# Kernel tuning notes

Measured on AMD Instinct MI355X. Metric: run time of the kernel, lower is better.

## Reference

```python
import jax, jax.numpy as jnp
import numpy as np

B, H, S, D = 2, 16, 2048, 64

def setup_inputs() -> dict:
    key0 = jax.random.key(0)
    kq, kk, kv = jax.random.split(key0, 3)
    return {
        "query": jax.random.normal(kq, (B, H, S, D), dtype=jnp.float32),
        "key": jax.random.normal(kk, (B, H, S, D), dtype=jnp.float32),
        "value": jax.random.normal(kv, (B, H, S, D), dtype=jnp.float32),
        "inv_scale_factor": jnp.full((1,), np.sqrt(D), dtype=jnp.float32),
    }

def reference(query, key, value, inv_scale_factor):
    # qk: [B,H,S,S]
    qk = jnp.einsum("bhqd,bhkd->bhqk", query, key)
    scaled_qk = qk / inv_scale_factor
    softmax_qk = jax.nn.softmax(scaled_qk, axis=-1)
    # dropout_p = 0.0 -> identity (deterministic reference)
    out = jnp.einsum("bhqk,bhkd->bhqd", softmax_qk, value)
    return out
```

## Files before the change

kernel.cpp:

```cpp
#include <hip/hip_runtime.h>
#include <hip/hip_bf16.h>


typedef __attribute__((ext_vector_type(8))) short short8;
typedef __attribute__((ext_vector_type(4))) float floatx4;

#define NB 2
#define NH 16
#define SS 2048
#define DD 64

#define QM 64
#define KN 64
#define NITER (SS / KN)

#define LOG2E 1.44269504f

#define MFMA16(a, b, c) __builtin_amdgcn_mfma_f32_16x16x32_bf16(a, b, c, 0, 0, 0)
#define WAIT_LGKM0() __builtin_amdgcn_s_waitcnt(0x007F)

#define KF_SHORTS (32 * 32 * 2 * 2 * 2 * 64 * 8)
#define VF_SHORTS (32 * 32 * 2 * 4 * 64 * 8)

static __device__ inline unsigned pack2bf(float a, float b) {
    unsigned ua = __builtin_bit_cast(unsigned, a) + 0x8000u;
    unsigned ub = __builtin_bit_cast(unsigned, b) + 0x8000u;
    return __builtin_amdgcn_perm(ub, ua, 0x07060302u);
}

static __device__ inline unsigned cvtpk(float lo, float hi) {
    unsigned r;
    asm("v_cvt_pk_bf16_f32 %0, %1, %2" : "=v"(r) : "v"(lo), "v"(hi));
    return r;
}

static __device__ inline int swz(int row, int col) {
    return row * 64 + ((((col >> 3) ^ row) & 7) << 3) + (col & 7);
}

__global__ __launch_bounds__(256)
void prepack_kernel(const float* __restrict__ K, const float* __restrict__ V,
                    short* __restrict__ Kf, short* __restrict__ Vf)
{
    int t = blockIdx.x * 256 + threadIdx.x;
    if (t < 524288) {
        int lane = t & 63, rest = t >> 6;
        int ks = rest & 1, nt = (rest >> 1) & 1, wn = (rest >> 2) & 1;
        int hk = rest >> 3;
        int n_g = hk * 64 + wn * 32 + nt * 16 + (lane & 15);
        int d   = ks * 32 + ((lane >> 4) << 3);
        const float* src = K + (size_t)n_g * DD + d;
        float4 f0 = *(const float4*)src;
        float4 f1 = *(const float4*)(src + 4);
        uint4 o;
        o.x = pack2bf(f0.x, f0.y); o.y = pack2bf(f0.z, f0.w);
        o.z = pack2bf(f1.x, f1.y); o.w = pack2bf(f1.z, f1.w);
        *(uint4*)(Kf + (size_t)t * 8) = o;
    } else {
        int u = t - 524288;
        int lane = u & 63, rest = u >> 6;
        int dt = rest & 3, wn = (rest >> 2) & 1;
        int hk = rest >> 3;
        int d  = dt * 16 + (lane & 15);
        int n0 = hk * 64 + wn * 32 + ((lane >> 4) << 3);
        const float* src = V + (size_t)n0 * DD + d;
        float v[8];
#pragma unroll
        for (int jj = 0; jj < 8; ++jj) v[jj] = src[(size_t)jj * DD];
        uint4 o;
        o.x = pack2bf(v[0], v[1]); o.y = pack2bf(v[2], v[3]);
        o.z = pack2bf(v[4], v[5]); o.w = pack2bf(v[6], v[7]);
        *(uint4*)(Vf + (size_t)u * 8) = o;
    }
}

__global__ __launch_bounds__(256, 4)
void fattn_kernel(const float* __restrict__ Q, const short* __restrict__ Kf,
                  const short* __restrict__ Vf, const float* __restrict__ isf,
                  float* __restrict__ O)
{
    __shared__ __align__(16) char smem[17664];
    short* P_lds = (short*)smem;
    float* O_buf = (float*)smem;
    float* l_buf = (float*)(smem + 17408);
#define OSTR 68

    const int tid  = threadIdx.x;
    const int wave = tid >> 6;
    const int w_m  = wave & 1;
    const int w_n  = wave >> 1;
    const int lane = tid & 63;
    const int l15  = lane & 15;
    const int quad = lane >> 4;

    const int b    = blockIdx.x & 1023;
    const int xcd  = b & 7;
    const int j    = b >> 3;
    const int head = xcd + 8 * (j & 3);
    const int qt   = j >> 2;

    const float scl2 = (1.0f / isf[0]) * LOG2E;

    const float* Qh = Q + (size_t)head * SS * DD;
    float*       Oh = O + (size_t)head * SS * DD;

    const short* kp = Kf + (size_t)head * 131072 + w_n * 2048 + lane * 8;
    const short* vp = Vf + (size_t)head * 131072 + w_n * 2048 + lane * 8;

    short8 kA0 = *(const short8*)(kp + 0);
    short8 kA1 = *(const short8*)(kp + 512);
    short8 kA2 = *(const short8*)(kp + 1024);
    short8 kA3 = *(const short8*)(kp + 1536);
    short8 kB0, kB1, kB2, kB3;

    short8 q_frag[2][2];
#pragma unroll
    for (int mt = 0; mt < 2; ++mt) {
        const float* qrow = Qh + (size_t)(qt * QM + w_m * 32 + mt * 16 + l15) * DD;
#pragma unroll
        for (int ks = 0; ks < 2; ++ks) {
            float4 f0 = *(const float4*)(qrow + ks * 32 + quad * 8);
            float4 f1 = *(const float4*)(qrow + ks * 32 + quad * 8 + 4);
            uint4 qp;
            qp.x = pack2bf(f0.x * scl2, f0.y * scl2);
            qp.y = pack2bf(f0.z * scl2, f0.w * scl2);
            qp.z = pack2bf(f1.x * scl2, f1.y * scl2);
            qp.w = pack2bf(f1.z * scl2, f1.w * scl2);
            q_frag[mt][ks] = __builtin_bit_cast(short8, qp);
        }
    }

    floatx4 o_acc[2][4];
#pragma unroll
    for (int mt = 0; mt < 2; ++mt)
#pragma unroll
        for (int dt = 0; dt < 4; ++dt)
#pragma unroll
            for (int i = 0; i < 4; ++i) o_acc[mt][dt][i] = 0.0f;

    float lsum[2] = {0.0f, 0.0f};

    short* pw[2][2];
    const short* pr[2];
#pragma unroll
    for (int mt = 0; mt < 2; ++mt) {
        const int m = w_m * 32 + mt * 16 + l15;
#pragma unroll
        for (int nt = 0; nt < 2; ++nt)
            pw[mt][nt] = &P_lds[swz(m, w_n * 32 + nt * 16 + quad * 4)];
        pr[mt] = &P_lds[swz(m, w_n * 32 + quad * 8)];
    }

#define SOFTMAX_ST(sv, mt, nt)                                        \
    do {                                                              \
        float p0 = __builtin_amdgcn_exp2f((sv)[0]);                   \
        float p1 = __builtin_amdgcn_exp2f((sv)[1]);                   \
        float p2 = __builtin_amdgcn_exp2f((sv)[2]);                   \
        float p3 = __builtin_amdgcn_exp2f((sv)[3]);                   \
        uint2 pk; pk.x = cvtpk(p0, p1); pk.y = cvtpk(p2, p3);         \
        *(uint2*)pw[mt][nt] = pk;                                     \
        lsum[mt] += (p0 + p1) + (p2 + p3);                            \
    } while (0)

#define FATTN_BODY(K0, K1, K2, K3, V0, V1, V2, V3)                    \
    do {                                                              \
        floatx4 s00 = {0.f, 0.f, 0.f, 0.f};                           \
        floatx4 s01 = s00, s10 = s00, s11 = s00;                      \
        s00 = MFMA16(K0, q_frag[0][0], s00);                          \
        s10 = MFMA16(K0, q_frag[1][0], s10);                          \
        s01 = MFMA16(K2, q_frag[0][0], s01);                          \
        s11 = MFMA16(K2, q_frag[1][0], s11);                          \
        s00 = MFMA16(K1, q_frag[0][1], s00);                          \
        s10 = MFMA16(K1, q_frag[1][1], s10);                          \
        s01 = MFMA16(K3, q_frag[0][1], s01);                          \
        s11 = MFMA16(K3, q_frag[1][1], s11);                          \
        SOFTMAX_ST(s00, 0, 0);                                        \
        SOFTMAX_ST(s10, 1, 0);                                        \
        SOFTMAX_ST(s01, 0, 1);                                        \
        SOFTMAX_ST(s11, 1, 1);                                        \
        WAIT_LGKM0();    \
        short8 pf0 = *(const short8*)pr[0];                           \
        short8 pf1 = *(const short8*)pr[1];                           \
        o_acc[0][0] = MFMA16(V0, pf0, o_acc[0][0]);                   \
        o_acc[0][1] = MFMA16(V1, pf0, o_acc[0][1]);                   \
        o_acc[0][2] = MFMA16(V2, pf0, o_acc[0][2]);                   \
        o_acc[0][3] = MFMA16(V3, pf0, o_acc[0][3]);                   \
        o_acc[1][0] = MFMA16(V0, pf1, o_acc[1][0]);                   \
        o_acc[1][1] = MFMA16(V1, pf1, o_acc[1][1]);                   \
        o_acc[1][2] = MFMA16(V2, pf1, o_acc[1][2]);                   \
        o_acc[1][3] = MFMA16(V3, pf1, o_acc[1][3]);                   \
    } while (0)

    for (int kb = 0; kb < NITER; kb += 2) {
        short8 v0 = *(const short8*)(vp + 0);
        short8 v1 = *(const short8*)(vp + 512);
        short8 v2 = *(const short8*)(vp + 1024);
        short8 v3 = *(const short8*)(vp + 1536);
        kB0 = *(const short8*)(kp + 4096);
        kB1 = *(const short8*)(kp + 4608);
        kB2 = *(const short8*)(kp + 5120);
        kB3 = *(const short8*)(kp + 5632);
        FATTN_BODY(kA0, kA1, kA2, kA3, v0, v1, v2, v3);

        short8 w0 = *(const short8*)(vp + 4096);
        short8 w1 = *(const short8*)(vp + 4608);
        short8 w2 = *(const short8*)(vp + 5120);
        short8 w3 = *(const short8*)(vp + 5632);
        kA0 = *(const short8*)(kp + 8192);
        kA1 = *(const short8*)(kp + 8704);
        kA2 = *(const short8*)(kp + 9216);
        kA3 = *(const short8*)(kp + 9728);
        FATTN_BODY(kB0, kB1, kB2, kB3, w0, w1, w2, w3);

        kp += 8192; vp += 8192;
    }

#pragma unroll
    for (int mt = 0; mt < 2; ++mt) {
        lsum[mt] += __shfl_xor(lsum[mt], 16);
        lsum[mt] += __shfl_xor(lsum[mt], 32);
    }
    __syncthreads();

    if (w_n == 1) {
#pragma unroll
        for (int mt = 0; mt < 2; ++mt) {
            const int orow = (w_m * 32 + mt * 16 + l15) * OSTR;
#pragma unroll
            for (int dt = 0; dt < 4; ++dt) {
                float4 v = { o_acc[mt][dt][0], o_acc[mt][dt][1],
                             o_acc[mt][dt][2], o_acc[mt][dt][3] };
                *(float4*)&O_buf[orow + dt * 16 + quad * 4] = v;
            }
            if (quad == 0) l_buf[w_m * 32 + mt * 16 + l15] = lsum[mt];
        }
    }
    __syncthreads();
    if (w_n == 0) {
#pragma unroll
        for (int mt = 0; mt < 2; ++mt) {
            const int m_blk = w_m * 32 + mt * 16 + l15;
            float lt = lsum[mt] + l_buf[m_blk];
            float rl = 1.0f / lt;
            float* orow = Oh + (size_t)(qt * QM + m_blk) * DD;
#pragma unroll
            for (int dt = 0; dt < 4; ++dt) {
                float4 part = *(float4*)&O_buf[m_blk * OSTR + dt * 16 + quad * 4];
                float4 v;
                v.x = (o_acc[mt][dt][0] + part.x) * rl;
                v.y = (o_acc[mt][dt][1] + part.y) * rl;
                v.z = (o_acc[mt][dt][2] + part.z) * rl;
                v.w = (o_acc[mt][dt][3] + part.w) * rl;
                *(float4*)(orow + dt * 16 + quad * 4) = v;
            }
        }
    }
}

extern "C" void kernel_launch(void* const* d_in, const int* in_sizes, int n_in,
                              void* d_out, int out_size, void* d_ws, size_t ws_size,
                              hipStream_t stream) {
    const float* Q   = (const float*)d_in[0];
    const float* K   = (const float*)d_in[1];
    const float* V   = (const float*)d_in[2];
    const float* isf = (const float*)d_in[3];
    float* O = (float*)d_out;

    short* Kf = (short*)d_ws;
    short* Vf = Kf + KF_SHORTS;

    prepack_kernel<<<4096, 256, 0, stream>>>(K, V, Kf, Vf);
    fattn_kernel<<<1024, 256, 0, stream>>>(Q, Kf, Vf, isf, O);
}
```

Measured before the change: 139.5 us.

## Switch attention to 32x32x16 MFMA and pass P through lane shuffles instead of LDS

```diff
diff --git a/kernel.cpp b/kernel.cpp
--- a/kernel.cpp
+++ b/kernel.cpp
@@ -3,24 +3,17 @@
 
 
 typedef __attribute__((ext_vector_type(8))) short short8;
-typedef __attribute__((ext_vector_type(4))) float floatx4;
-
-#define NB 2
-#define NH 16
+typedef __attribute__((ext_vector_type(16))) float floatx16;
+
 #define SS 2048
 #define DD 64
-
-#define QM 64
-#define KN 64
-#define NITER (SS / KN)
-
+#define NITER (SS / 64)
 #define LOG2E 1.44269504f
 
-#define MFMA16(a, b, c) __builtin_amdgcn_mfma_f32_16x16x32_bf16(a, b, c, 0, 0, 0)
-#define WAIT_LGKM0() __builtin_amdgcn_s_waitcnt(0x007F)
-
-#define KF_SHORTS (32 * 32 * 2 * 2 * 2 * 64 * 8)
-#define VF_SHORTS (32 * 32 * 2 * 4 * 64 * 8)
+#define MFMA32(a, b, c) __builtin_amdgcn_mfma_f32_32x32x16_bf16(a, b, c, 0, 0, 0)
+
+#define KF_SHORTS (32 * 64 * 4 * 64 * 8)
+#define VF_SHORTS (32 * 64 * 4 * 64 * 8)
 
 static __device__ inline unsigned pack2bf(float a, float b) {
     unsigned ua = __builtin_bit_cast(unsigned, a) + 0x8000u;
@@ -32,10 +25,6 @@
     unsigned r;
     asm("v_cvt_pk_bf16_f32 %0, %1, %2" : "=v"(r) : "v"(lo), "v"(hi));
     return r;
-}
-
-static __device__ inline int swz(int row, int col) {
-    return row * 64 + ((((col >> 3) ^ row) & 7) << 3) + (col & 7);
 }
 
 __global__ __launch_bounds__(256)
@@ -43,13 +32,13 @@
                     short* __restrict__ Kf, short* __restrict__ Vf)
 {
     int t = blockIdx.x * 256 + threadIdx.x;
+    int lane = t & 63;
+    int l31 = lane & 31, hi = lane >> 5;
     if (t < 524288) {
-        int lane = t & 63, rest = t >> 6;
-        int ks = rest & 1, nt = (rest >> 1) & 1, wn = (rest >> 2) & 1;
-        int hk = rest >> 3;
-        int n_g = hk * 64 + wn * 32 + nt * 16 + (lane & 15);
-        int d   = ks * 32 + ((lane >> 4) << 3);
-        const float* src = K + (size_t)n_g * DD + d;
+        int c = t >> 6;
+        int ks = c & 3, kvb = (c >> 2) & 63, hd = c >> 8;
+        const float* src = K + (size_t)hd * 131072
+                             + (size_t)(kvb * 32 + l31) * 64 + ks * 16 + hi * 8;
         float4 f0 = *(const float4*)src;
         float4 f1 = *(const float4*)(src + 4);
         uint4 o;
@@ -58,15 +47,14 @@
         *(uint4*)(Kf + (size_t)t * 8) = o;
     } else {
         int u = t - 524288;
-        int lane = u & 63, rest = u >> 6;
-        int dt = rest & 3, wn = (rest >> 2) & 1;
-        int hk = rest >> 3;
-        int d  = dt * 16 + (lane & 15);
-        int n0 = hk * 64 + wn * 32 + ((lane >> 4) << 3);
-        const float* src = V + (size_t)n0 * DD + d;
+        int c = u >> 6;
+        int ksl = c & 1, dt = (c >> 1) & 1, kvb = (c >> 2) & 63, hd = c >> 8;
+        const float* src = V + (size_t)hd * 131072
+                             + (size_t)(kvb * 32 + ksl * 16 + hi * 8) * 64
+                             + dt * 32 + l31;
         float v[8];
 #pragma unroll
-        for (int jj = 0; jj < 8; ++jj) v[jj] = src[(size_t)jj * DD];
+        for (int jj = 0; jj < 8; ++jj) v[jj] = src[(size_t)jj * 64];
         uint4 o;
         o.x = pack2bf(v[0], v[1]); o.y = pack2bf(v[2], v[3]);
         o.z = pack2bf(v[4], v[5]); o.w = pack2bf(v[6], v[7]);
@@ -80,7 +68,6 @@
                   float* __restrict__ O)
 {
     __shared__ __align__(16) char smem[17664];
-    short* P_lds = (short*)smem;
     float* O_buf = (float*)smem;
     float* l_buf = (float*)(smem + 17408);
 #define OSTR 68
@@ -90,8 +77,8 @@
     const int w_m  = wave & 1;
     const int w_n  = wave >> 1;
     const int lane = tid & 63;
-    const int l15  = lane & 15;
-    const int quad = lane >> 4;
+    const int l31  = lane & 31;
+    const int hi   = lane >> 5;
 
     const int b    = blockIdx.x & 1023;
     const int xcd  = b & 7;
@@ -113,147 +100,117 @@
     short8 kA3 = *(const short8*)(kp + 1536);
     short8 kB0, kB1, kB2, kB3;
 
-    short8 q_frag[2][2];
-#pragma unroll
-    for (int mt = 0; mt < 2; ++mt) {
-        const float* qrow = Qh + (size_t)(qt * QM + w_m * 32 + mt * 16 + l15) * DD;
-#pragma unroll
-        for (int ks = 0; ks < 2; ++ks) {
-            float4 f0 = *(const float4*)(qrow + ks * 32 + quad * 8);
-            float4 f1 = *(const float4*)(qrow + ks * 32 + quad * 8 + 4);
+    short8 q_frag[4];
+    {
+        const float* qrow = Qh + (size_t)(qt * 64 + w_m * 32 + l31) * DD;
+#pragma unroll
+        for (int ks = 0; ks < 4; ++ks) {
+            float4 f0 = *(const float4*)(qrow + ks * 16 + hi * 8);
+            float4 f1 = *(const float4*)(qrow + ks * 16 + hi * 8 + 4);
             uint4 qp;
             qp.x = pack2bf(f0.x * scl2, f0.y * scl2);
             qp.y = pack2bf(f0.z * scl2, f0.w * scl2);
             qp.z = pack2bf(f1.x * scl2, f1.y * scl2);
             qp.w = pack2bf(f1.z * scl2, f1.w * scl2);
-            q_frag[mt][ks] = __builtin_bit_cast(short8, qp);
+            q_frag[ks] = __builtin_bit_cast(short8, qp);
         }
     }
 
-    floatx4 o_acc[2][4];
-#pragma unroll
-    for (int mt = 0; mt < 2; ++mt)
-#pragma unroll
-        for (int dt = 0; dt < 4; ++dt)
-#pragma unroll
-            for (int i = 0; i < 4; ++i) o_acc[mt][dt][i] = 0.0f;
-
-    float lsum[2] = {0.0f, 0.0f};
-
-    short* pw[2][2];
-    const short* pr[2];
-#pragma unroll
-    for (int mt = 0; mt < 2; ++mt) {
-        const int m = w_m * 32 + mt * 16 + l15;
-#pragma unroll
-        for (int nt = 0; nt < 2; ++nt)
-            pw[mt][nt] = &P_lds[swz(m, w_n * 32 + nt * 16 + quad * 4)];
-        pr[mt] = &P_lds[swz(m, w_n * 32 + quad * 8)];
-    }
-
-#define SOFTMAX_ST(sv, mt, nt)                                        \
-    do {                                                              \
-        float p0 = __builtin_amdgcn_exp2f((sv)[0]);                   \
-        float p1 = __builtin_amdgcn_exp2f((sv)[1]);                   \
-        float p2 = __builtin_amdgcn_exp2f((sv)[2]);                   \
-        float p3 = __builtin_amdgcn_exp2f((sv)[3]);                   \
-        uint2 pk; pk.x = cvtpk(p0, p1); pk.y = cvtpk(p2, p3);         \
-        *(uint2*)pw[mt][nt] = pk;                                     \
-        lsum[mt] += (p0 + p1) + (p2 + p3);                            \
+    floatx16 o_acc[2];
+#pragma unroll
+    for (int i = 0; i < 16; ++i) { o_acc[0][i] = 0.0f; o_acc[1][i] = 0.0f; }
+    float lsum = 0.0f;
+
+#define FBODY(K0, K1, K2, K3, V00, V01, V10, V11)                          \
+    do {                                                                   \
+        floatx16 s = {0.f,0.f,0.f,0.f,0.f,0.f,0.f,0.f,                     \
+                      0.f,0.f,0.f,0.f,0.f,0.f,0.f,0.f};                    \
+        s = MFMA32(K0, q_frag[0], s);                                      \
+        s = MFMA32(K1, q_frag[1], s);                                      \
+        s = MFMA32(K2, q_frag[2], s);                                      \
+        s = MFMA32(K3, q_frag[3], s);                                      \
+        float p[16];                                                       \
+        _Pragma("unroll")                                                  \
+        for (int i = 0; i < 16; ++i) p[i] = __builtin_amdgcn_exp2f(s[i]);  \
+        lsum += (((p[0]+p[1])+(p[2]+p[3]))+((p[4]+p[5])+(p[6]+p[7])))      \
+              + (((p[8]+p[9])+(p[10]+p[11]))+((p[12]+p[13])+(p[14]+p[15])));\
+         \
+        unsigned x0 = cvtpk(p[0], p[1]),   x1 = cvtpk(p[2], p[3]);         \
+        unsigned y0 = cvtpk(p[4], p[5]),   y1 = cvtpk(p[6], p[7]);         \
+        unsigned x2 = cvtpk(p[8], p[9]),   x3 = cvtpk(p[10], p[11]);       \
+        unsigned y2 = cvtpk(p[12], p[13]), y3 = cvtpk(p[14], p[15]);       \
+                              \
+        unsigned f0 = __shfl_xor(hi ? x0 : y0, 32);                        \
+        unsigned f1 = __shfl_xor(hi ? x1 : y1, 32);                        \
+        unsigned f2 = __shfl_xor(hi ? x2 : y2, 32);                        \
+        unsigned f3 = __shfl_xor(hi ? x3 : y3, 32);                        \
+        uint4 B0u = { hi ? f0 : x0, hi ? f1 : x1,                          \
+                      hi ? y0 : f0, hi ? y1 : f1 };    \
+        uint4 B1u = { hi ? f2 : x2, hi ? f3 : x3,                          \
+                      hi ? y2 : f2, hi ? y3 : f3 };   \
+        short8 Bf0 = __builtin_bit_cast(short8, B0u);                      \
+        short8 Bf1 = __builtin_bit_cast(short8, B1u);                      \
+        o_acc[0] = MFMA32(V00, Bf0, o_acc[0]);                             \
+        o_acc[1] = MFMA32(V10, Bf0, o_acc[1]);                             \
+        o_acc[0] = MFMA32(V01, Bf1, o_acc[0]);                             \
+        o_acc[1] = MFMA32(V11, Bf1, o_acc[1]);                             \
     } while (0)
 
-#define FATTN_BODY(K0, K1, K2, K3, V0, V1, V2, V3)                    \
-    do {                                                              \
-        floatx4 s00 = {0.f, 0.f, 0.f, 0.f};                           \
-        floatx4 s01 = s00, s10 = s00, s11 = s00;                      \
-        s00 = MFMA16(K0, q_frag[0][0], s00);                          \
-        s10 = MFMA16(K0, q_frag[1][0], s10);                          \
-        s01 = MFMA16(K2, q_frag[0][0], s01);                          \
-        s11 = MFMA16(K2, q_frag[1][0], s11);                          \
-        s00 = MFMA16(K1, q_frag[0][1], s00);                          \
-        s10 = MFMA16(K1, q_frag[1][1], s10);                          \
-        s01 = MFMA16(K3, q_frag[0][1], s01);                          \
-        s11 = MFMA16(K3, q_frag[1][1], s11);                          \
-        SOFTMAX_ST(s00, 0, 0);                                        \
-        SOFTMAX_ST(s10, 1, 0);                                        \
-        SOFTMAX_ST(s01, 0, 1);                                        \
-        SOFTMAX_ST(s11, 1, 1);                                        \
-        WAIT_LGKM0();    \
-        short8 pf0 = *(const short8*)pr[0];                           \
-        short8 pf1 = *(const short8*)pr[1];                           \
-        o_acc[0][0] = MFMA16(V0, pf0, o_acc[0][0]);                   \
-        o_acc[0][1] = MFMA16(V1, pf0, o_acc[0][1]);                   \
-        o_acc[0][2] = MFMA16(V2, pf0, o_acc[0][2]);                   \
-        o_acc[0][3] = MFMA16(V3, pf0, o_acc[0][3]);                   \
-        o_acc[1][0] = MFMA16(V0, pf1, o_acc[1][0]);                   \
-        o_acc[1][1] = MFMA16(V1, pf1, o_acc[1][1]);                   \
-        o_acc[1][2] = MFMA16(V2, pf1, o_acc[1][2]);                   \
-        o_acc[1][3] = MFMA16(V3, pf1, o_acc[1][3]);                   \
-    } while (0)
-
     for (int kb = 0; kb < NITER; kb += 2) {
-        short8 v0 = *(const short8*)(vp + 0);
-        short8 v1 = *(const short8*)(vp + 512);
-        short8 v2 = *(const short8*)(vp + 1024);
-        short8 v3 = *(const short8*)(vp + 1536);
+        short8 v00 = *(const short8*)(vp + 0);
+        short8 v01 = *(const short8*)(vp + 512);
+        short8 v10 = *(const short8*)(vp + 1024);
+        short8 v11 = *(const short8*)(vp + 1536);
         kB0 = *(const short8*)(kp + 4096);
         kB1 = *(const short8*)(kp + 4608);
         kB2 = *(const short8*)(kp + 5120);
         kB3 = *(const short8*)(kp + 5632);
-        FATTN_BODY(kA0, kA1, kA2, kA3, v0, v1, v2, v3);
-
-        short8 w0 = *(const short8*)(vp + 4096);
-        short8 w1 = *(const short8*)(vp + 4608);
-        short8 w2 = *(const short8*)(vp + 5120);
-        short8 w3 = *(const short8*)(vp + 5632);
+        FBODY(kA0, kA1, kA2, kA3, v00, v01, v10, v11);
+
+        short8 w00 = *(const short8*)(vp + 4096);
+        short8 w01 = *(const short8*)(vp + 4608);
+        short8 w10 = *(const short8*)(vp + 5120);
+        short8 w11 = *(const short8*)(vp + 5632);
         kA0 = *(const short8*)(kp + 8192);
         kA1 = *(const short8*)(kp + 8704);
         kA2 = *(const short8*)(kp + 9216);
         kA3 = *(const short8*)(kp + 9728);
-        FATTN_BODY(kB0, kB1, kB2, kB3, w0, w1, w2, w3);
+        FBODY(kB0, kB1, kB2, kB3, w00, w01, w10, w11);
 
         kp += 8192; vp += 8192;
     }
 
-#pragma unroll
-    for (int mt = 0; mt < 2; ++mt) {
-        lsum[mt] += __shfl_xor(lsum[mt], 16);
-        lsum[mt] += __shfl_xor(lsum[mt], 32);
-    }
-    __syncthreads();
-
+    lsum += __shfl_xor(lsum, 32);
+
+    const int row = w_m * 32 + l31;
     if (w_n == 1) {
 #pragma unroll
-        for (int mt = 0; mt < 2; ++mt) {
-            const int orow = (w_m * 32 + mt * 16 + l15) * OSTR;
-#pragma unroll
-            for (int dt = 0; dt < 4; ++dt) {
-                float4 v = { o_acc[mt][dt][0], o_acc[mt][dt][1],
-                             o_acc[mt][dt][2], o_acc[mt][dt][3] };
-                *(float4*)&O_buf[orow + dt * 16 + quad * 4] = v;
+        for (int dt = 0; dt < 2; ++dt)
+#pragma unroll
+            for (int g = 0; g < 4; ++g) {
+                float4 v = { o_acc[dt][g * 4 + 0], o_acc[dt][g * 4 + 1],
+                             o_acc[dt][g * 4 + 2], o_acc[dt][g * 4 + 3] };
+                *(float4*)&O_buf[row * OSTR + dt * 32 + g * 8 + hi * 4] = v;
             }
-            if (quad == 0) l_buf[w_m * 32 + mt * 16 + l15] = lsum[mt];
-        }
+        if (lane < 32) l_buf[row] = lsum;
     }
     __syncthreads();
     if (w_n == 0) {
-#pragma unroll
-        for (int mt = 0; mt < 2; ++mt) {
-            const int m_blk = w_m * 32 + mt * 16 + l15;
-            float lt = lsum[mt] + l_buf[m_blk];
-            float rl = 1.0f / lt;
-            float* orow = Oh + (size_t)(qt * QM + m_blk) * DD;
-#pragma unroll
-            for (int dt = 0; dt < 4; ++dt) {
-                float4 part = *(float4*)&O_buf[m_blk * OSTR + dt * 16 + quad * 4];
+        float lt = lsum + l_buf[row];
+        float rl = 1.0f / lt;
+        float* orow = Oh + (size_t)(qt * 64 + row) * DD;
+#pragma unroll
+        for (int dt = 0; dt < 2; ++dt)
+#pragma unroll
+            for (int g = 0; g < 4; ++g) {
+                float4 part = *(float4*)&O_buf[row * OSTR + dt * 32 + g * 8 + hi * 4];
                 float4 v;
-                v.x = (o_acc[mt][dt][0] + part.x) * rl;
-                v.y = (o_acc[mt][dt][1] + part.y) * rl;
-                v.z = (o_acc[mt][dt][2] + part.z) * rl;
-                v.w = (o_acc[mt][dt][3] + part.w) * rl;
-                *(float4*)(orow + dt * 16 + quad * 4) = v;
+                v.x = (o_acc[dt][g * 4 + 0] + part.x) * rl;
+                v.y = (o_acc[dt][g * 4 + 1] + part.y) * rl;
+                v.z = (o_acc[dt][g * 4 + 2] + part.z) * rl;
+                v.w = (o_acc[dt][g * 4 + 3] + part.w) * rl;
+                *(float4*)(orow + dt * 32 + g * 8 + hi * 4) = v;
             }
-        }
     }
 }
 
```

Result: slower. 159.1 us (+14.0%).
